# Kernel tuning notes

Measured on AMD Instinct MI355X. Metric: run time of the kernel, lower is better.

The kernel has to match this reference:

```python
import jax, jax.numpy as jnp
import numpy as np

N, E, H, F_IN, F_OUT = 100000, 1600000, 4, 128, 32
SLOPE = 0.2


def setup_inputs() -> dict:
    key = jax.random.key(0)
    ks = jax.random.split(key, 5)
    x = jax.random.normal(ks[0], (N, F_IN), dtype=jnp.float32)
    edge_src = jax.random.randint(ks[1], (E,), 0, N)
    edge_dst = jax.random.randint(ks[2], (E,), 0, N)
    # xavier-ish init (gain 1.414) as in reset_parameters
    weight = jax.random.normal(ks[3], (H, F_IN, F_OUT), dtype=jnp.float32) * (1.414 / np.sqrt(F_IN))
    a = jax.random.normal(ks[4], (H, 2 * F_OUT), dtype=jnp.float32) * (1.414 / np.sqrt(2 * F_OUT))
    bias = jnp.zeros((H, F_OUT), dtype=jnp.float32)
    return {"x": x, "weight": weight, "a": a, "bias": bias,
            "edge_src": edge_src, "edge_dst": edge_dst}


def reference(x, weight, a, bias, edge_src, edge_dst):
    # per-head linear transform: [N,H,F_OUT]
    h = jnp.einsum('nf,hfo->nho', x, weight)
    # split attention vector: e_ij = LeakyReLU(a_src.h_i + a_dst.h_j)
    a_src, a_dst = a[:, :F_OUT], a[:, F_OUT:]
    alpha_src = jnp.einsum('nho,ho->nh', h, a_src)  # [N,H]
    alpha_dst = jnp.einsum('nho,ho->nh', h, a_dst)  # [N,H]
    e = jax.nn.leaky_relu(alpha_src[edge_src] + alpha_dst[edge_dst], SLOPE)  # [E,H]
    # numerically-stable edge softmax over incoming edges of each dst node
    e_max = jax.ops.segment_max(e, edge_dst, num_segments=N)  # [N,H]
    e_max = jnp.where(jnp.isfinite(e_max), e_max, 0.0)        # nodes with no in-edges
    e_exp = jnp.exp(e - e_max[edge_dst])                      # [E,H]
    denom = jax.ops.segment_sum(e_exp, edge_dst, num_segments=N)  # [N,H]
    att = e_exp / (denom[edge_dst] + 1e-16)                   # [E,H]
    # weighted aggregation: out[j] = sum_i att_ij * h_i
    msg = h[edge_src] * att[:, :, None]                       # [E,H,F_OUT]
    out = jax.ops.segment_sum(msg, edge_dst, num_segments=N)  # [N,H,F_OUT]
    out = out + bias                                          # broadcast [H,F_OUT]
    return out.reshape(N, H * F_OUT)                          # multi-head concat
```

## Files before the change

kernel.cpp:

```cpp
#include <hip/hip_runtime.h>

#define NN   100000
#define NE   1600000
#define NH   4
#define FIN  128
#define FOUT 32
#define HF   128
#define SLOPE 0.2f

#define PBKT  64
#define PNB   ((NN+PBKT-1)/PBKT)
#define CAP   2048
#define NMF   1563
#define NPART 391
#define DSLOT 48

typedef __attribute__((ext_vector_type(8))) short short8v;
typedef __attribute__((ext_vector_type(4))) float f32x4;

__device__ __forceinline__ unsigned int bpack(float lo, float hi){
    unsigned int ul = __float_as_uint(lo), uh = __float_as_uint(hi);
    ul = (ul + 0x7fffu + ((ul>>16)&1u)) >> 16;
    uh = (uh + 0x7fffu + ((uh>>16)&1u)) >> 16;
    return ul | (uh<<16);
}
__device__ __forceinline__ short bf16of(float f){
    unsigned int u = __float_as_uint(f);
    return (short)((u + 0x7fffu + ((u>>16)&1u)) >> 16);
}
__device__ __forceinline__ float blo(unsigned int u){ return __uint_as_float(u<<16); }
__device__ __forceinline__ float bhi(unsigned int u){ return __uint_as_float(u&0xffff0000u); }

__global__ __launch_bounds__(1024) void prep_k(
    const float* __restrict__ w, const float* __restrict__ a,
    short* __restrict__ wfrag, short* __restrict__ wafrag,
    int* __restrict__ cnt)
{
    __shared__ float wal[1024];
    int t = threadIdx.x;
    {
        int s = t>>7, f = t&127, h = s&3;
        const float* ap = a + h*64 + (s>>2)*32;
        const float* wp = w + (size_t)h*4096 + f*32;
        float acc = 0.f;
        #pragma unroll
        for (int o=0;o<32;o++) acc = fmaf(wp[o], ap[o], acc);
        wal[s*128 + f] = acc;
    }
    __syncthreads();
    for (int idx=t; idx<2048; idx+=1024){
        int lane = idx&63, ks=(idx>>6)&3, cf=(idx>>8)&1, wvv=idx>>9;
        int col = wvv*32 + cf*16 + (lane&15);
        int fb  = ks*32 + (lane>>4)*8;
        const float* wp = w + (size_t)(col>>5)*4096 + (col&31);
        short8v bv;
        #pragma unroll
        for (int j=0;j<8;j++) bv[j] = bf16of(wp[(size_t)(fb+j)*32]);
        ((short8v*)wfrag)[idx] = bv;
    }
    if (t < 256){
        int lane = t&63, ks = t>>6;
        int l15 = lane&15, fb = ks*32 + (lane>>4)*8;
        short8v bv;
        #pragma unroll
        for (int j=0;j<8;j++) bv[j] = (l15<8) ? bf16of(wal[l15*128 + fb + j]) : (short)0;
        ((short8v*)wafrag)[t] = bv;
    }
    for (int i=t;i<PNB;i+=1024) cnt[i]=0;
}

__global__ __launch_bounds__(256) void fused_k(
    const float* __restrict__ x, const short* __restrict__ wfrag,
    const short* __restrict__ wafrag, unsigned int* __restrict__ hb,
    float* __restrict__ asrc, float* __restrict__ adst,
    const int* __restrict__ esrc, const int* __restrict__ edst,
    int* __restrict__ cnt, unsigned int* __restrict__ parr)
{
    __shared__ char smem[16384];
    const int bid = blockIdx.x;
    const int t   = threadIdx.x;
    const int r5  = bid % 5;

    if (r5 == 4){
        int* hist = (int*)smem;
        int* bcur = hist + PNB;
        for (int i=t;i<PNB;i+=256) hist[i]=0;
        __syncthreads();
        int base = (bid/5)*4096;
        #pragma unroll
        for (int k=0;k<16;k++){
            int e = base + k*256 + t;
            if (e < NE) atomicAdd(&hist[edst[e]>>6], 1);
        }
        __syncthreads();
        for (int i=t;i<PNB;i+=256)
            bcur[i] = hist[i] ? atomicAdd(&cnt[i], hist[i]) : 0;
        __syncthreads();
        #pragma unroll
        for (int k=0;k<16;k++){
            int e = base + k*256 + t;
            if (e < NE){
                int d = edst[e], s = esrc[e];
                int pos = atomicAdd(&bcur[d>>6], 1);
                parr[(size_t)(d>>6)*CAP + pos] = ((unsigned int)s<<6) | (unsigned int)(d & 63);
            }
        }
        return;
    }

    const int mi = (bid/5)*4 + r5;
    if (mi >= NMF) return;
    char* lds = smem;
    const int n0 = mi*64;

    #pragma unroll
    for (int p=0; p<8; ++p){
        int r  = p*8 + (t>>5);
        int cq = t & 31;
        int nr = n0 + r; if (nr > NN-1) nr = NN-1;
        float4 v = *(const float4*)(x + (size_t)nr*FIN + cq*4);
        unsigned int lo = bpack(v.x, v.y), hi = bpack(v.z, v.w);
        int cb = (cq*8) ^ ((r&7)<<4);
        *(uint2*)(lds + r*256 + cb) = make_uint2(lo, hi);
    }
    __syncthreads();

    const int wv   = t>>6;
    const int lane = t&63;
    const int l15  = lane&15;
    const int lk   = (lane>>4)<<3;

    short8v Bf[3][4];
    const short8v* wf  = (const short8v*)wfrag;
    const short8v* waf = (const short8v*)wafrag;
    #pragma unroll
    for (int cf=0; cf<2; ++cf)
        #pragma unroll
        for (int ks=0; ks<4; ++ks)
            Bf[cf][ks] = wf[((wv*2+cf)*4+ks)*64 + lane];
    if (wv==0){
        #pragma unroll
        for (int ks=0; ks<4; ++ks) Bf[2][ks] = waf[ks*64 + lane];
    }

    f32x4 C[4][3];
    #pragma unroll
    for (int rt=0;rt<4;rt++)
        #pragma unroll
        for (int cf=0;cf<3;cf++){ f32x4 z = {0.f,0.f,0.f,0.f}; C[rt][cf] = z; }

    const int axor = (lane&7)<<4;
    #pragma unroll
    for (int rt=0; rt<4; ++rt){
        int row = rt*16 + l15;
        const char* arow = lds + row*256;
        short8v Af[4];
        #pragma unroll
        for (int ks=0; ks<4; ++ks)
            Af[ks] = *(const short8v*)(arow + (((ks<<6) | (lk<<1)) ^ axor));
        #pragma unroll
        for (int ks=0; ks<4; ++ks){
            C[rt][0] = __builtin_amdgcn_mfma_f32_16x16x32_bf16(Af[ks], Bf[0][ks], C[rt][0], 0,0,0);
            C[rt][1] = __builtin_amdgcn_mfma_f32_16x16x32_bf16(Af[ks], Bf[1][ks], C[rt][1], 0,0,0);
            if (wv==0)
                C[rt][2] = __builtin_amdgcn_mfma_f32_16x16x32_bf16(Af[ks], Bf[2][ks], C[rt][2], 0,0,0);
        }
    }

    const int g4 = l15>>2;
    #pragma unroll
    for (int rt=0; rt<4; ++rt){
        #pragma unroll
        for (int cf=0; cf<2; ++cf){
            f32x4 c = C[rt][cf];
            #pragma unroll
            for (int i=0;i<4;i++){
                float v1 = __shfl_xor(c[i], 1);
                float v2 = __shfl_xor(c[i], 2);
                float v3 = __shfl_xor(c[i], 3);
                int node = n0 + rt*16 + ((lane>>4)<<2) + i;
                if ((l15&3)==0 && node < NN){
                    uint2 pk = make_uint2(bpack(c[i], v1), bpack(v2, v3));
                    *(uint2*)(hb + (size_t)node*64 + wv*16 + cf*8 + g4*2) = pk;
                }
            }
        }
    }
    if (wv==0 && l15 < 8){
        #pragma unroll
        for (int rt=0; rt<4; ++rt){
            f32x4 c = C[rt][2];
            #pragma unroll
            for (int i=0;i<4;i++){
                int node = n0 + rt*16 + ((lane>>4)<<2) + i;
                if (node < NN){
                    if (l15 < 4) asrc[(size_t)node*4 + l15]     = c[i];
                    else         adst[(size_t)node*4 + (l15-4)] = c[i];
                }
            }
        }
    }
}

__global__ __launch_bounds__(256) void gather_k(
    const int* __restrict__ cnt,
    const unsigned int* __restrict__ parr,
    const float* __restrict__ asrc, const float* __restrict__ adst,
    const unsigned int* __restrict__ hb, const float* __restrict__ bias,
    float* __restrict__ out)
{
    __shared__ int lcur[PBKT];
    __shared__ int lcsr[PBKT*DSLOT];
    const int bkt = blockIdx.x;
    const int t = threadIdx.x;
    int cb = cnt[bkt]; if (cb > CAP) cb = CAP;
    const unsigned int* pb = parr + (size_t)bkt*CAP;

    if (t < PBKT) lcur[t] = 0;
    __syncthreads();
    for (int i=t; i<cb; i+=256){
        unsigned int en = pb[i];
        int dl = (int)(en & 63u);
        int pos = atomicAdd(&lcur[dl], 1);
        if (pos < DSLOT) lcsr[dl*DSLOT + pos] = (int)(en >> 6);
    }
    __syncthreads();

    const int wv   = t>>6;
    const int lane = t&63;
    const int q    = lane>>4;
    const int l15  = lane&15;
    const int head = l15>>2;
    const uint4* hb4 = (const uint4*)hb;
    const float4 bi0 = *(const float4*)(bias + 8*l15);
    const float4 bi1 = *(const float4*)(bias + 8*l15 + 4);

    for (int dl = wv; dl < PBKT; dl += 4){
        int d = bkt*PBKT + dl;
        if (d >= NN) break;
        int m = lcur[dl]; if (m > DSLOT) m = DSLOT;
        const int base = dl*DSLOT;

        float ad_h = adst[(size_t)d*NH + head];
        float ssum = 0.f;
        float ac0=0.f, ac1=0.f, ac2=0.f, ac3=0.f, ac4=0.f, ac5=0.f, ac6=0.f, ac7=0.f;

        int k = 0;
        for (; k + 8 <= m; k += 8){
            int sA = lcsr[base+k+q];
            int sB = lcsr[base+k+4+q];
            float aA = asrc[(size_t)sA*NH+head];
            float aB = asrc[(size_t)sB*NH+head];
            uint4 uA = hb4[(size_t)sA*16 + l15];
            uint4 uB = hb4[(size_t)sB*16 + l15];
            float vA=aA+ad_h; vA=fmaxf(vA,SLOPE*vA); float pA=__expf(vA);
            float vB=aB+ad_h; vB=fmaxf(vB,SLOPE*vB); float pB=__expf(vB);
            ssum += pA + pB;
            ac0 = fmaf(pA,blo(uA.x), fmaf(pB,blo(uB.x), ac0));
            ac1 = fmaf(pA,bhi(uA.x), fmaf(pB,bhi(uB.x), ac1));
            ac2 = fmaf(pA,blo(uA.y), fmaf(pB,blo(uB.y), ac2));
            ac3 = fmaf(pA,bhi(uA.y), fmaf(pB,bhi(uB.y), ac3));
            ac4 = fmaf(pA,blo(uA.z), fmaf(pB,blo(uB.z), ac4));
            ac5 = fmaf(pA,bhi(uA.z), fmaf(pB,bhi(uB.z), ac5));
            ac6 = fmaf(pA,blo(uA.w), fmaf(pB,blo(uB.w), ac6));
            ac7 = fmaf(pA,bhi(uA.w), fmaf(pB,bhi(uB.w), ac7));
        }
        for (; k < m; k += 4){
            int r = m - k;
            if (q < r){
                int s = lcsr[base+k+q];
                float a0 = asrc[(size_t)s*NH+head];
                uint4 u = hb4[(size_t)s*16 + l15];
                float v = a0 + ad_h; v = fmaxf(v, SLOPE*v);
                float p = __expf(v);
                ssum += p;
                ac0 = fmaf(p, blo(u.x), ac0);
                ac1 = fmaf(p, bhi(u.x), ac1);
                ac2 = fmaf(p, blo(u.y), ac2);
                ac3 = fmaf(p, bhi(u.y), ac3);
                ac4 = fmaf(p, blo(u.z), ac4);
                ac5 = fmaf(p, bhi(u.z), ac5);
                ac6 = fmaf(p, blo(u.w), ac6);
                ac7 = fmaf(p, bhi(u.w), ac7);
            }
        }
        ssum += __shfl_xor(ssum, 16); ssum += __shfl_xor(ssum, 32);
        ac0 += __shfl_xor(ac0, 16); ac0 += __shfl_xor(ac0, 32);
        ac1 += __shfl_xor(ac1, 16); ac1 += __shfl_xor(ac1, 32);
        ac2 += __shfl_xor(ac2, 16); ac2 += __shfl_xor(ac2, 32);
        ac3 += __shfl_xor(ac3, 16); ac3 += __shfl_xor(ac3, 32);
        ac4 += __shfl_xor(ac4, 16); ac4 += __shfl_xor(ac4, 32);
        ac5 += __shfl_xor(ac5, 16); ac5 += __shfl_xor(ac5, 32);
        ac6 += __shfl_xor(ac6, 16); ac6 += __shfl_xor(ac6, 32);
        ac7 += __shfl_xor(ac7, 16); ac7 += __shfl_xor(ac7, 32);
        if (q == 0){
            float inv = 1.f / (ssum + 1e-16f);
            float4 o0 = make_float4(ac0*inv + bi0.x, ac1*inv + bi0.y,
                                    ac2*inv + bi0.z, ac3*inv + bi0.w);
            float4 o1 = make_float4(ac4*inv + bi1.x, ac5*inv + bi1.y,
                                    ac6*inv + bi1.z, ac7*inv + bi1.w);
            float* op = out + (size_t)d*HF + 8*l15;
            *(float4*)op     = o0;
            *(float4*)(op+4) = o1;
        }
    }
}

extern "C" void kernel_launch(void* const* d_in, const int* in_sizes, int n_in,
                              void* d_out, int out_size, void* d_ws, size_t ws_size,
                              hipStream_t stream)
{
    const float* x    = (const float*)d_in[0];
    const float* w    = (const float*)d_in[1];
    const float* a    = (const float*)d_in[2];
    const float* bias = (const float*)d_in[3];
    const int* esrc   = (const int*)d_in[4];
    const int* edst   = (const int*)d_in[5];
    float* out = (float*)d_out;

    short* wfrag  = (short*)d_ws;
    short* wafrag = wfrag + 16384;
    unsigned int* hb = (unsigned int*)(wafrag + 2048);
    float* as   = (float*)(hb + (size_t)NN*64);
    float* ad   = as + (size_t)NN*NH;
    unsigned int* parr = (unsigned int*)(ad + (size_t)NN*NH);
    int* cnt    = (int*)(parr + (size_t)PNB*CAP);

    hipLaunchKernelGGL(prep_k, dim3(1), dim3(1024), 0, stream,
                       w, a, wfrag, wafrag, cnt);
    hipLaunchKernelGGL(fused_k, dim3(NMF + NPART + 1), dim3(256), 0, stream,
                       x, wfrag, wafrag, hb, as, ad, esrc, edst, cnt, parr);
    hipLaunchKernelGGL(gather_k, dim3(PNB), dim3(256), 0, stream,
                       cnt, parr, as, ad, hb, bias, out);
}
```

Baseline: 128.9 us.

## Split each gather bucket across four blocks and unroll edge loop by sixteen

Each 64-destination bucket now goes to four blocks, each handling 16 destinations, so the gather kernel launches four times as many blocks with less shared memory per block. Every block still scans the whole bucket's edge list and keeps only its quarter, which quadruples reads of the partition array. The inner edge loop adds a 16-edge unrolled stage that issues more independent hb loads per iteration, aiming for more memory-level parallelism.

```diff
diff --git a/kernel.cpp b/kernel.cpp
--- a/kernel.cpp
+++ b/kernel.cpp
@@ -202,6 +202,14 @@
     }
 }
 
+#define EDGE_ACC(s, p) do{                                             \
+    uint4 _u = hb4[(size_t)(s)*16 + l15];                              \
+    ac0 = fmaf((p), blo(_u.x), ac0); ac1 = fmaf((p), bhi(_u.x), ac1);  \
+    ac2 = fmaf((p), blo(_u.y), ac2); ac3 = fmaf((p), bhi(_u.y), ac3);  \
+    ac4 = fmaf((p), blo(_u.z), ac4); ac5 = fmaf((p), bhi(_u.z), ac5);  \
+    ac6 = fmaf((p), blo(_u.w), ac6); ac7 = fmaf((p), bhi(_u.w), ac7);  \
+}while(0)
+
 __global__ __launch_bounds__(256) void gather_k(
     const int* __restrict__ cnt,
     const unsigned int* __restrict__ parr,
@@ -209,20 +217,23 @@
     const unsigned int* __restrict__ hb, const float* __restrict__ bias,
     float* __restrict__ out)
 {
-    __shared__ int lcur[PBKT];
-    __shared__ int lcsr[PBKT*DSLOT];
-    const int bkt = blockIdx.x;
+    __shared__ int lcur[16];
+    __shared__ int lcsr[16*DSLOT];
+    const int blk = blockIdx.x;
+    const int bkt = blk >> 2, qb = blk & 3;
     const int t = threadIdx.x;
     int cb = cnt[bkt]; if (cb > CAP) cb = CAP;
     const unsigned int* pb = parr + (size_t)bkt*CAP;
 
-    if (t < PBKT) lcur[t] = 0;
+    if (t < 16) lcur[t] = 0;
     __syncthreads();
     for (int i=t; i<cb; i+=256){
         unsigned int en = pb[i];
         int dl = (int)(en & 63u);
-        int pos = atomicAdd(&lcur[dl], 1);
-        if (pos < DSLOT) lcsr[dl*DSLOT + pos] = (int)(en >> 6);
+        if ((dl>>4) == qb){
+            int pos = atomicAdd(&lcur[dl & 15], 1);
+            if (pos < DSLOT) lcsr[(dl&15)*DSLOT + pos] = (int)(en >> 6);
+        }
     }
     __syncthreads();
 
@@ -235,8 +246,10 @@
     const float4 bi0 = *(const float4*)(bias + 8*l15);
     const float4 bi1 = *(const float4*)(bias + 8*l15 + 4);
 
-    for (int dl = wv; dl < PBKT; dl += 4){
-        int d = bkt*PBKT + dl;
+    #pragma unroll
+    for (int i=0; i<4; ++i){
+        int dl = wv*4 + i;
+        int d = bkt*PBKT + qb*16 + dl;
         if (d >= NN) break;
         int m = lcur[dl]; if (m > DSLOT) m = DSLOT;
         const int base = dl*DSLOT;
@@ -246,42 +259,34 @@
         float ac0=0.f, ac1=0.f, ac2=0.f, ac3=0.f, ac4=0.f, ac5=0.f, ac6=0.f, ac7=0.f;
 
         int k = 0;
+        for (; k + 16 <= m; k += 16){
+            int s0 = lcsr[base+k   +q], s1 = lcsr[base+k+4 +q];
+            int s2 = lcsr[base+k+8 +q], s3 = lcsr[base+k+12+q];
+            float a0 = asrc[(size_t)s0*NH+head], a1 = asrc[(size_t)s1*NH+head];
+            float a2 = asrc[(size_t)s2*NH+head], a3 = asrc[(size_t)s3*NH+head];
+            float v0=a0+ad_h; v0=fmaxf(v0,SLOPE*v0); float p0=__expf(v0);
+            float v1=a1+ad_h; v1=fmaxf(v1,SLOPE*v1); float p1=__expf(v1);
+            float v2=a2+ad_h; v2=fmaxf(v2,SLOPE*v2); float p2=__expf(v2);
+            float v3=a3+ad_h; v3=fmaxf(v3,SLOPE*v3); float p3=__expf(v3);
+            ssum += (p0+p1)+(p2+p3);
+            EDGE_ACC(s0,p0); EDGE_ACC(s1,p1); EDGE_ACC(s2,p2); EDGE_ACC(s3,p3);
+        }
         for (; k + 8 <= m; k += 8){
-            int sA = lcsr[base+k+q];
-            int sB = lcsr[base+k+4+q];
-            float aA = asrc[(size_t)sA*NH+head];
-            float aB = asrc[(size_t)sB*NH+head];
-            uint4 uA = hb4[(size_t)sA*16 + l15];
-            uint4 uB = hb4[(size_t)sB*16 + l15];
-            float vA=aA+ad_h; vA=fmaxf(vA,SLOPE*vA); float pA=__expf(vA);
-            float vB=aB+ad_h; vB=fmaxf(vB,SLOPE*vB); float pB=__expf(vB);
-            ssum += pA + pB;
-            ac0 = fmaf(pA,blo(uA.x), fmaf(pB,blo(uB.x), ac0));
-            ac1 = fmaf(pA,bhi(uA.x), fmaf(pB,bhi(uB.x), ac1));
-            ac2 = fmaf(pA,blo(uA.y), fmaf(pB,blo(uB.y), ac2));
-            ac3 = fmaf(pA,bhi(uA.y), fmaf(pB,bhi(uB.y), ac3));
-            ac4 = fmaf(pA,blo(uA.z), fmaf(pB,blo(uB.z), ac4));
-            ac5 = fmaf(pA,bhi(uA.z), fmaf(pB,bhi(uB.z), ac5));
-            ac6 = fmaf(pA,blo(uA.w), fmaf(pB,blo(uB.w), ac6));
-            ac7 = fmaf(pA,bhi(uA.w), fmaf(pB,bhi(uB.w), ac7));
+            int s0 = lcsr[base+k+q], s1 = lcsr[base+k+4+q];
+            float a0 = asrc[(size_t)s0*NH+head], a1 = asrc[(size_t)s1*NH+head];
+            float v0=a0+ad_h; v0=fmaxf(v0,SLOPE*v0); float p0=__expf(v0);
+            float v1=a1+ad_h; v1=fmaxf(v1,SLOPE*v1); float p1=__expf(v1);
+            ssum += p0 + p1;
+            EDGE_ACC(s0,p0); EDGE_ACC(s1,p1);
         }
         for (; k < m; k += 4){
             int r = m - k;
             if (q < r){
-                int s = lcsr[base+k+q];
-                float a0 = asrc[(size_t)s*NH+head];
-                uint4 u = hb4[(size_t)s*16 + l15];
-                float v = a0 + ad_h; v = fmaxf(v, SLOPE*v);
-                float p = __expf(v);
-                ssum += p;
-                ac0 = fmaf(p, blo(u.x), ac0);
-                ac1 = fmaf(p, bhi(u.x), ac1);
-                ac2 = fmaf(p, blo(u.y), ac2);
-                ac3 = fmaf(p, bhi(u.y), ac3);
-                ac4 = fmaf(p, blo(u.z), ac4);
-                ac5 = fmaf(p, bhi(u.z), ac5);
-                ac6 = fmaf(p, blo(u.w), ac6);
-                ac7 = fmaf(p, bhi(u.w), ac7);
+                int s0 = lcsr[base+k+q];
+                float a0 = asrc[(size_t)s0*NH+head];
+                float v0=a0+ad_h; v0=fmaxf(v0,SLOPE*v0); float p0=__expf(v0);
+                ssum += p0;
+                EDGE_ACC(s0,p0);
             }
         }
         ssum += __shfl_xor(ssum, 16); ssum += __shfl_xor(ssum, 32);
@@ -330,6 +335,6 @@
                        w, a, wfrag, wafrag, cnt);
     hipLaunchKernelGGL(fused_k, dim3(NMF + NPART + 1), dim3(256), 0, stream,
                        x, wfrag, wafrag, hb, as, ad, esrc, edst, cnt, parr);
-    hipLaunchKernelGGL(gather_k, dim3(PNB), dim3(256), 0, stream,
+    hipLaunchKernelGGL(gather_k, dim3(PNB*4), dim3(256), 0, stream,
                        cnt, parr, as, ad, hb, bias, out);
 }
```

Result: no change. 130.5 us (+1.2%).

## Process two node tiles per GEMM block and two destinations per gather wave

Applied to the files above, without the earlier changes.

The fused transform kernel now handles two 64-node tiles per block. It loads the second tile's x rows into registers while the first tile's MFMAs run, using double-buffered LDS, and interleaves blocks 2:1 with the edge-partition blocks. The gather kernel has each wave accumulate two destination nodes together (dl and dl+32), which doubles the independent hb/asrc loads in flight. The intent is to hide global-memory latency in both stages. The cost is twice the LDS per fused block, more registers in gather, and fewer blocks overall.

```diff
diff --git a/kernel.cpp b/kernel.cpp
--- a/kernel.cpp
+++ b/kernel.cpp
@@ -12,6 +12,7 @@
 #define PNB   ((NN+PBKT-1)/PBKT)
 #define CAP   2048
 #define NMF   1563
+#define NMFB  782
 #define NPART 391
 #define DSLOT 48
 
@@ -69,6 +70,67 @@
     for (int i=t;i<PNB;i+=1024) cnt[i]=0;
 }
 
+#define STAGE_TILE(n0, ldsb) do{                                          \
+    _Pragma("unroll")                                                     \
+    for (int p=0; p<8; ++p){                                              \
+        int r  = p*8 + (t>>5); int cq = t & 31;                           \
+        int nr = (n0) + r; if (nr > NN-1) nr = NN-1;                      \
+        float4 v = *(const float4*)(x + (size_t)nr*FIN + cq*4);           \
+        int cb = (cq*8) ^ ((r&7)<<4);                                     \
+        *(uint2*)((ldsb) + r*256 + cb) =                                  \
+            make_uint2(bpack(v.x,v.y), bpack(v.z,v.w));                   \
+    } }while(0)
+
+#define ZERO_C() do{                                                      \
+    _Pragma("unroll") for (int rt=0;rt<4;rt++)                            \
+    _Pragma("unroll") for (int cf=0;cf<3;cf++){                           \
+        f32x4 z = {0.f,0.f,0.f,0.f}; C[rt][cf] = z; } }while(0)
+
+#define DO_MFMA(ldsb) do{                                                 \
+    _Pragma("unroll")                                                     \
+    for (int rt=0; rt<4; ++rt){                                           \
+        int row = rt*16 + l15;                                            \
+        const char* arow = (ldsb) + row*256;                              \
+        short8v Af[4];                                                    \
+        _Pragma("unroll")                                                 \
+        for (int ks=0; ks<4; ++ks)                                        \
+            Af[ks] = *(const short8v*)(arow + (((ks<<6)|(lk<<1)) ^ axor));\
+        _Pragma("unroll")                                                 \
+        for (int ks=0; ks<4; ++ks){                                       \
+            C[rt][0] = __builtin_amdgcn_mfma_f32_16x16x32_bf16(Af[ks], Bf[0][ks], C[rt][0], 0,0,0); \
+            C[rt][1] = __builtin_amdgcn_mfma_f32_16x16x32_bf16(Af[ks], Bf[1][ks], C[rt][1], 0,0,0); \
+            if (wv==0)                                                    \
+                C[rt][2] = __builtin_amdgcn_mfma_f32_16x16x32_bf16(Af[ks], Bf[2][ks], C[rt][2], 0,0,0); \
+        } } }while(0)
+
+#define EPILOGUE(n0) do{                                                  \
+    _Pragma("unroll")                                                     \
+    for (int rt=0; rt<4; ++rt){                                           \
+        _Pragma("unroll")                                                 \
+        for (int cf=0; cf<2; ++cf){                                       \
+            f32x4 c = C[rt][cf];                                          \
+            _Pragma("unroll")                                             \
+            for (int i=0;i<4;i++){                                        \
+                float v1 = __shfl_xor(c[i], 1);                           \
+                float v2 = __shfl_xor(c[i], 2);                           \
+                float v3 = __shfl_xor(c[i], 3);                           \
+                int node = (n0) + rt*16 + ((lane>>4)<<2) + i;             \
+                if ((l15&3)==0 && node < NN){                             \
+                    uint2 pk = make_uint2(bpack(c[i], v1), bpack(v2, v3));\
+                    *(uint2*)(hb + (size_t)node*64 + wv*16 + cf*8 + g4*2) = pk; \
+                } } } }                                                   \
+    if (wv==0 && l15 < 8){                                                \
+        _Pragma("unroll")                                                 \
+        for (int rt=0; rt<4; ++rt){                                       \
+            f32x4 c = C[rt][2];                                           \
+            _Pragma("unroll")                                             \
+            for (int i=0;i<4;i++){                                        \
+                int node = (n0) + rt*16 + ((lane>>4)<<2) + i;             \
+                if (node < NN){                                           \
+                    if (l15 < 4) asrc[(size_t)node*4 + l15]     = c[i];   \
+                    else         adst[(size_t)node*4 + (l15-4)] = c[i];   \
+                } } } } }while(0)
+
 __global__ __launch_bounds__(256) void fused_k(
     const float* __restrict__ x, const short* __restrict__ wfrag,
     const short* __restrict__ wafrag, unsigned int* __restrict__ hb,
@@ -76,17 +138,16 @@
     const int* __restrict__ esrc, const int* __restrict__ edst,
     int* __restrict__ cnt, unsigned int* __restrict__ parr)
 {
-    __shared__ char smem[16384];
+    __shared__ __align__(16) char smem[32768];
     const int bid = blockIdx.x;
     const int t   = threadIdx.x;
-    const int r5  = bid % 5;
-
-    if (r5 == 4){
+
+    if (bid % 3 == 2){
         int* hist = (int*)smem;
         int* bcur = hist + PNB;
         for (int i=t;i<PNB;i+=256) hist[i]=0;
         __syncthreads();
-        int base = (bid/5)*4096;
+        int base = (bid/3)*4096;
         #pragma unroll
         for (int k=0;k<16;k++){
             int e = base + k*256 + t;
@@ -108,27 +169,21 @@
         return;
     }
 
-    const int mi = (bid/5)*4 + r5;
-    if (mi >= NMF) return;
-    char* lds = smem;
-    const int n0 = mi*64;
-
-    #pragma unroll
-    for (int p=0; p<8; ++p){
-        int r  = p*8 + (t>>5);
-        int cq = t & 31;
-        int nr = n0 + r; if (nr > NN-1) nr = NN-1;
-        float4 v = *(const float4*)(x + (size_t)nr*FIN + cq*4);
-        unsigned int lo = bpack(v.x, v.y), hi = bpack(v.z, v.w);
-        int cb = (cq*8) ^ ((r&7)<<4);
-        *(uint2*)(lds + r*256 + cb) = make_uint2(lo, hi);
-    }
-    __syncthreads();
+    const int mIdx = (bid/3)*2 + (bid%3);
+    const int mi0 = mIdx*2, mi1 = mi0 + 1;
+    const bool has1 = (mi1 < NMF);
+    char* buf0 = smem;
+    char* buf1 = smem + 16384;
 
     const int wv   = t>>6;
     const int lane = t&63;
     const int l15  = lane&15;
     const int lk   = (lane>>4)<<3;
+    const int axor = (lane&7)<<4;
+    const int g4   = l15>>2;
+
+    STAGE_TILE(mi0*64, buf0);
+    __syncthreads();
 
     short8v Bf[3][4];
     const short8v* wf  = (const short8v*)wfrag;
@@ -138,69 +193,98 @@
         #pragma unroll
         for (int ks=0; ks<4; ++ks)
             Bf[cf][ks] = wf[((wv*2+cf)*4+ks)*64 + lane];
-    if (wv==0){
-        #pragma unroll
-        for (int ks=0; ks<4; ++ks) Bf[2][ks] = waf[ks*64 + lane];
+    #pragma unroll
+    for (int ks=0; ks<4; ++ks) Bf[2][ks] = waf[ks*64 + lane];
+
+    float4 xr0,xr1,xr2,xr3,xr4,xr5,xr6,xr7;
+    if (has1){
+        const int cq = t&31;
+        #define LOADX(p, dst) { int r=(p)*8+(t>>5); int nr=mi1*64+r; if(nr>NN-1)nr=NN-1; \
+                                dst = *(const float4*)(x + (size_t)nr*FIN + cq*4); }
+        LOADX(0,xr0) LOADX(1,xr1) LOADX(2,xr2) LOADX(3,xr3)
+        LOADX(4,xr4) LOADX(5,xr5) LOADX(6,xr6) LOADX(7,xr7)
+        #undef LOADX
     }
 
     f32x4 C[4][3];
-    #pragma unroll
-    for (int rt=0;rt<4;rt++)
-        #pragma unroll
-        for (int cf=0;cf<3;cf++){ f32x4 z = {0.f,0.f,0.f,0.f}; C[rt][cf] = z; }
-
-    const int axor = (lane&7)<<4;
-    #pragma unroll
-    for (int rt=0; rt<4; ++rt){
-        int row = rt*16 + l15;
-        const char* arow = lds + row*256;
-        short8v Af[4];
-        #pragma unroll
-        for (int ks=0; ks<4; ++ks)
-            Af[ks] = *(const short8v*)(arow + (((ks<<6) | (lk<<1)) ^ axor));
-        #pragma unroll
-        for (int ks=0; ks<4; ++ks){
-            C[rt][0] = __builtin_amdgcn_mfma_f32_16x16x32_bf16(Af[ks], Bf[0][ks], C[rt][0], 0,0,0);
-            C[rt][1] = __builtin_amdgcn_mfma_f32_16x16x32_bf16(Af[ks], Bf[1][ks], C[rt][1], 0,0,0);
-            if (wv==0)
-                C[rt][2] = __builtin_amdgcn_mfma_f32_16x16x32_bf16(Af[ks], Bf[2][ks], C[rt][2], 0,0,0);
-        }
-    }
-
-    const int g4 = l15>>2;
-    #pragma unroll
-    for (int rt=0; rt<4; ++rt){
-        #pragma unroll
-        for (int cf=0; cf<2; ++cf){
-            f32x4 c = C[rt][cf];
-            #pragma unroll
-            for (int i=0;i<4;i++){
-                float v1 = __shfl_xor(c[i], 1);
-                float v2 = __shfl_xor(c[i], 2);
-                float v3 = __shfl_xor(c[i], 3);
-                int node = n0 + rt*16 + ((lane>>4)<<2) + i;
-                if ((l15&3)==0 && node < NN){
-                    uint2 pk = make_uint2(bpack(c[i], v1), bpack(v2, v3));
-                    *(uint2*)(hb + (size_t)node*64 + wv*16 + cf*8 + g4*2) = pk;
-                }
-            }
-        }
-    }
-    if (wv==0 && l15 < 8){
-        #pragma unroll
-        for (int rt=0; rt<4; ++rt){
-            f32x4 c = C[rt][2];
-            #pragma unroll
-            for (int i=0;i<4;i++){
-                int node = n0 + rt*16 + ((lane>>4)<<2) + i;
-                if (node < NN){
-                    if (l15 < 4) asrc[(size_t)node*4 + l15]     = c[i];
-                    else         adst[(size_t)node*4 + (l15-4)] = c[i];
-                }
-            }
-        }
-    }
-}
+    ZERO_C();
+    DO_MFMA(buf0);
+
+    if (has1){
+        const int cq = t&31;
+        #define WRX(p, src) { int r=(p)*8+(t>>5); int cb=(cq*8)^((r&7)<<4); \
+            *(uint2*)(buf1 + r*256 + cb) = make_uint2(bpack(src.x,src.y), bpack(src.z,src.w)); }
+        WRX(0,xr0) WRX(1,xr1) WRX(2,xr2) WRX(3,xr3)
+        WRX(4,xr4) WRX(5,xr5) WRX(6,xr6) WRX(7,xr7)
+        #undef WRX
+    }
+
+    EPILOGUE(mi0*64);
+    __syncthreads();
+
+    if (has1){
+        ZERO_C();
+        DO_MFMA(buf1);
+        EPILOGUE(mi1*64);
+    }
+}
+
+#define ACC2(x0,x1,u0,u1,adh,ss,ac) do{                                   \
+    float _v0=(x0)+(adh); _v0=fmaxf(_v0,SLOPE*_v0); float _p0=__expf(_v0);\
+    float _v1=(x1)+(adh); _v1=fmaxf(_v1,SLOPE*_v1); float _p1=__expf(_v1);\
+    ss += _p0+_p1;                                                        \
+    ac[0]=fmaf(_p0,blo(u0.x),fmaf(_p1,blo(u1.x),ac[0]));                  \
+    ac[1]=fmaf(_p0,bhi(u0.x),fmaf(_p1,bhi(u1.x),ac[1]));                  \
+    ac[2]=fmaf(_p0,blo(u0.y),fmaf(_p1,blo(u1.y),ac[2]));                  \
+    ac[3]=fmaf(_p0,bhi(u0.y),fmaf(_p1,bhi(u1.y),ac[3]));                  \
+    ac[4]=fmaf(_p0,blo(u0.z),fmaf(_p1,blo(u1.z),ac[4]));                  \
+    ac[5]=fmaf(_p0,bhi(u0.z),fmaf(_p1,bhi(u1.z),ac[5]));                  \
+    ac[6]=fmaf(_p0,blo(u0.w),fmaf(_p1,blo(u1.w),ac[6]));                  \
+    ac[7]=fmaf(_p0,bhi(u0.w),fmaf(_p1,bhi(u1.w),ac[7])); }while(0)
+
+#define ACC1(x0,u0,adh,ss,ac) do{                                         \
+    float _v0=(x0)+(adh); _v0=fmaxf(_v0,SLOPE*_v0); float _p0=__expf(_v0);\
+    ss += _p0;                                                            \
+    ac[0]=fmaf(_p0,blo(u0.x),ac[0]); ac[1]=fmaf(_p0,bhi(u0.x),ac[1]);     \
+    ac[2]=fmaf(_p0,blo(u0.y),ac[2]); ac[3]=fmaf(_p0,bhi(u0.y),ac[3]);     \
+    ac[4]=fmaf(_p0,blo(u0.z),ac[4]); ac[5]=fmaf(_p0,bhi(u0.z),ac[5]);     \
+    ac[6]=fmaf(_p0,blo(u0.w),ac[6]); ac[7]=fmaf(_p0,bhi(u0.w),ac[7]); }while(0)
+
+#define DRAIN8(basek,kk,mm,adh,ss,ac)                                     \
+    for (; kk+8<=mm; kk+=8){                                              \
+        int _s0=lcsr[(basek)+kk+q], _s1=lcsr[(basek)+kk+4+q];             \
+        float _a0=asrc[(size_t)_s0*NH+head], _a1=asrc[(size_t)_s1*NH+head];\
+        uint4 _u0=hb4[(size_t)_s0*16+l15], _u1=hb4[(size_t)_s1*16+l15];   \
+        ACC2(_a0,_a1,_u0,_u1,adh,ss,ac);                                  \
+    }                                                                     \
+    for (; kk<mm; kk+=4){                                                 \
+        int _r=mm-kk;                                                     \
+        if (q<_r){                                                        \
+            int _s0=lcsr[(basek)+kk+q];                                   \
+            float _a0=asrc[(size_t)_s0*NH+head];                          \
+            uint4 _u0=hb4[(size_t)_s0*16+l15];                            \
+            ACC1(_a0,_u0,adh,ss,ac);                                      \
+        } }
+
+#define REDUCE_STORE(d,ss,ac) do{                                         \
+    ss += __shfl_xor(ss,16); ss += __shfl_xor(ss,32);                     \
+    ac[0]+=__shfl_xor(ac[0],16); ac[0]+=__shfl_xor(ac[0],32);             \
+    ac[1]+=__shfl_xor(ac[1],16); ac[1]+=__shfl_xor(ac[1],32);             \
+    ac[2]+=__shfl_xor(ac[2],16); ac[2]+=__shfl_xor(ac[2],32);             \
+    ac[3]+=__shfl_xor(ac[3],16); ac[3]+=__shfl_xor(ac[3],32);             \
+    ac[4]+=__shfl_xor(ac[4],16); ac[4]+=__shfl_xor(ac[4],32);             \
+    ac[5]+=__shfl_xor(ac[5],16); ac[5]+=__shfl_xor(ac[5],32);             \
+    ac[6]+=__shfl_xor(ac[6],16); ac[6]+=__shfl_xor(ac[6],32);             \
+    ac[7]+=__shfl_xor(ac[7],16); ac[7]+=__shfl_xor(ac[7],32);             \
+    if (q==0){                                                            \
+        float inv = 1.f/(ss + 1e-16f);                                    \
+        float4 o0 = make_float4(ac[0]*inv+bi0.x, ac[1]*inv+bi0.y,         \
+                                ac[2]*inv+bi0.z, ac[3]*inv+bi0.w);        \
+        float4 o1 = make_float4(ac[4]*inv+bi1.x, ac[5]*inv+bi1.y,         \
+                                ac[6]*inv+bi1.z, ac[7]*inv+bi1.w);        \
+        float* op = out + (size_t)(d)*HF + 8*l15;                         \
+        *(float4*)op = o0; *(float4*)(op+4) = o1;                         \
+    } }while(0)
 
 __global__ __launch_bounds__(256) void gather_k(
     const int* __restrict__ cnt,
@@ -235,74 +319,34 @@
     const float4 bi0 = *(const float4*)(bias + 8*l15);
     const float4 bi1 = *(const float4*)(bias + 8*l15 + 4);
 
-    for (int dl = wv; dl < PBKT; dl += 4){
-        int d = bkt*PBKT + dl;
-        if (d >= NN) break;
-        int m = lcur[dl]; if (m > DSLOT) m = DSLOT;
-        const int base = dl*DSLOT;
-
-        float ad_h = adst[(size_t)d*NH + head];
-        float ssum = 0.f;
-        float ac0=0.f, ac1=0.f, ac2=0.f, ac3=0.f, ac4=0.f, ac5=0.f, ac6=0.f, ac7=0.f;
-
-        int k = 0;
-        for (; k + 8 <= m; k += 8){
-            int sA = lcsr[base+k+q];
-            int sB = lcsr[base+k+4+q];
-            float aA = asrc[(size_t)sA*NH+head];
-            float aB = asrc[(size_t)sB*NH+head];
-            uint4 uA = hb4[(size_t)sA*16 + l15];
-            uint4 uB = hb4[(size_t)sB*16 + l15];
-            float vA=aA+ad_h; vA=fmaxf(vA,SLOPE*vA); float pA=__expf(vA);
-            float vB=aB+ad_h; vB=fmaxf(vB,SLOPE*vB); float pB=__expf(vB);
-            ssum += pA + pB;
-            ac0 = fmaf(pA,blo(uA.x), fmaf(pB,blo(uB.x), ac0));
-            ac1 = fmaf(pA,bhi(uA.x), fmaf(pB,bhi(uB.x), ac1));
-            ac2 = fmaf(pA,blo(uA.y), fmaf(pB,blo(uB.y), ac2));
-            ac3 = fmaf(pA,bhi(uA.y), fmaf(pB,bhi(uB.y), ac3));
-            ac4 = fmaf(pA,blo(uA.z), fmaf(pB,blo(uB.z), ac4));
-            ac5 = fmaf(pA,bhi(uA.z), fmaf(pB,bhi(uB.z), ac5));
-            ac6 = fmaf(pA,blo(uA.w), fmaf(pB,blo(uB.w), ac6));
-            ac7 = fmaf(pA,bhi(uA.w), fmaf(pB,bhi(uB.w), ac7));
+    for (int dl = wv; dl < 32; dl += 4){
+        int dA = bkt*PBKT + dl, dB = dA + 32;
+        bool vB = (dB < NN);
+        int mA = lcur[dl];      if (mA > DSLOT) mA = DSLOT;
+        int mB = vB ? lcur[dl+32] : 0; if (mB > DSLOT) mB = DSLOT;
+        const int baseA = dl*DSLOT, baseB = (dl+32)*DSLOT;
+        float adA = adst[(size_t)dA*NH + head];
+        float adB = vB ? adst[(size_t)dB*NH + head] : 0.f;
+        float sA = 0.f, sB = 0.f;
+        float aA[8] = {0.f,0.f,0.f,0.f,0.f,0.f,0.f,0.f};
+        float aB[8] = {0.f,0.f,0.f,0.f,0.f,0.f,0.f,0.f};
+
+        int kA = 0, kB = 0;
+        for (; kA+8 <= mA && kB+8 <= mB; kA += 8, kB += 8){
+            int sa0 = lcsr[baseA+kA+q],  sa1 = lcsr[baseA+kA+4+q];
+            int sb0 = lcsr[baseB+kB+q],  sb1 = lcsr[baseB+kB+4+q];
+            float xa0 = asrc[(size_t)sa0*NH+head], xa1 = asrc[(size_t)sa1*NH+head];
+            float xb0 = asrc[(size_t)sb0*NH+head], xb1 = asrc[(size_t)sb1*NH+head];
+            uint4 ua0 = hb4[(size_t)sa0*16+l15], ua1 = hb4[(size_t)sa1*16+l15];
+            uint4 ub0 = hb4[(size_t)sb0*16+l15], ub1 = hb4[(size_t)sb1*16+l15];
+            ACC2(xa0,xa1,ua0,ua1,adA,sA,aA);
+            ACC2(xb0,xb1,ub0,ub1,adB,sB,aB);
         }
-        for (; k < m; k += 4){
-            int r = m - k;
-            if (q < r){
-                int s = lcsr[base+k+q];
-                float a0 = asrc[(size_t)s*NH+head];
-                uint4 u = hb4[(size_t)s*16 + l15];
-                float v = a0 + ad_h; v = fmaxf(v, SLOPE*v);
-                float p = __expf(v);
-                ssum += p;
-                ac0 = fmaf(p, blo(u.x), ac0);
-                ac1 = fmaf(p, bhi(u.x), ac1);
-                ac2 = fmaf(p, blo(u.y), ac2);
-                ac3 = fmaf(p, bhi(u.y), ac3);
-                ac4 = fmaf(p, blo(u.z), ac4);
-                ac5 = fmaf(p, bhi(u.z), ac5);
-                ac6 = fmaf(p, blo(u.w), ac6);
-                ac7 = fmaf(p, bhi(u.w), ac7);
-            }
-        }
-        ssum += __shfl_xor(ssum, 16); ssum += __shfl_xor(ssum, 32);
-        ac0 += __shfl_xor(ac0, 16); ac0 += __shfl_xor(ac0, 32);
-        ac1 += __shfl_xor(ac1, 16); ac1 += __shfl_xor(ac1, 32);
-        ac2 += __shfl_xor(ac2, 16); ac2 += __shfl_xor(ac2, 32);
-        ac3 += __shfl_xor(ac3, 16); ac3 += __shfl_xor(ac3, 32);
-        ac4 += __shfl_xor(ac4, 16); ac4 += __shfl_xor(ac4, 32);
-        ac5 += __shfl_xor(ac5, 16); ac5 += __shfl_xor(ac5, 32);
-        ac6 += __shfl_xor(ac6, 16); ac6 += __shfl_xor(ac6, 32);
-        ac7 += __shfl_xor(ac7, 16); ac7 += __shfl_xor(ac7, 32);
-        if (q == 0){
-            float inv = 1.f / (ssum + 1e-16f);
-            float4 o0 = make_float4(ac0*inv + bi0.x, ac1*inv + bi0.y,
-                                    ac2*inv + bi0.z, ac3*inv + bi0.w);
-            float4 o1 = make_float4(ac4*inv + bi1.x, ac5*inv + bi1.y,
-                                    ac6*inv + bi1.z, ac7*inv + bi1.w);
-            float* op = out + (size_t)d*HF + 8*l15;
-            *(float4*)op     = o0;
-            *(float4*)(op+4) = o1;
-        }
+        DRAIN8(baseA,kA,mA,adA,sA,aA);
+        DRAIN8(baseB,kB,mB,adB,sB,aB);
+
+        REDUCE_STORE(dA,sA,aA);
+        if (vB) REDUCE_STORE(dB,sB,aB);
     }
 }
 
@@ -328,7 +372,7 @@
 
     hipLaunchKernelGGL(prep_k, dim3(1), dim3(1024), 0, stream,
                        w, a, wfrag, wafrag, cnt);
-    hipLaunchKernelGGL(fused_k, dim3(NMF + NPART + 1), dim3(256), 0, stream,
+    hipLaunchKernelGGL(fused_k, dim3(NMFB + NPART), dim3(256), 0, stream,
                        x, wfrag, wafrag, hb, as, ad, esrc, edst, cnt, parr);
     hipLaunchKernelGGL(gather_k, dim3(PNB), dim3(256), 0, stream,
                        cnt, parr, as, ad, hb, bias, out);
```

Result: slower. 136.3 us (+5.7%).
